# Kernel tuning notes

Measured on AMD Instinct MI355X. Metric: run time of the kernel, lower is better.

## Reference

```python
import jax, jax.numpy as jnp
import numpy as np

B, S, C, OUT = 8, 2048, 1024, 1024

def setup_inputs() -> dict:
    key = jax.random.key(0)
    ks = jax.random.split(key, 10)
    s = C ** -0.5
    return {
        "input": jax.random.normal(ks[0], (B, S, C), jnp.float32),
        "memory": jax.random.normal(ks[1], (B, S, C), jnp.float32),
        "Wq": jax.random.normal(ks[2], (C, C), jnp.float32) * s,
        "bq": jnp.zeros((C,), jnp.float32),
        "Wk": jax.random.normal(ks[3], (C, C), jnp.float32) * s,
        "bk": jnp.zeros((C,), jnp.float32),
        "Wv": jax.random.normal(ks[4], (C, C), jnp.float32) * s,
        "bv": jnp.zeros((C,), jnp.float32),
        "Wo": jax.random.normal(ks[5], (OUT, C), jnp.float32) * s,
        "bo": jnp.zeros((OUT,), jnp.float32),
    }

def reference(input, memory, Wq, bq, Wk, bk, Wv, bv, Wo, bo):
    depth_scale = input.shape[2] ** -0.5
    q = (input @ Wq.T + bq) * depth_scale          # [B, Sq, C]
    k = memory @ Wk.T + bk                          # [B, Sk, C]
    v = memory @ Wv.T + bv                          # [B, Sk, C]
    logit = jnp.einsum('bqc,bkc->bqk', q, k)        # [B, Sq, Sk]
    attn = jax.nn.softmax(logit, axis=-1)
    sel = jnp.einsum('bqk,bkc->bqc', attn, v)       # [B, Sq, C]
    return sel @ Wo.T + bo                          # [B, Sq, OUT]
```

## Files before the change

### kernel.cpp

```cpp
#include <hip/hip_runtime.h>
#include <hip/hip_bf16.h>


typedef __attribute__((ext_vector_type(8))) short short8;
typedef __attribute__((ext_vector_type(4))) float f32x4;

static __device__ __forceinline__ unsigned short f2bf(float f) {
  union { float f; unsigned u; } x; x.f = f;
  unsigned r = x.u + 0x7FFFu + ((x.u >> 16) & 1u);
  return (unsigned short)(r >> 16);
}

static __device__ __forceinline__ long long brickoff(int r_, int k_, int Kd) {
  return (long long)(r_ >> 7) * ((long long)128 * Kd) +
         (long long)(k_ >> 5) * 4096 +
         (r_ & 127) * 32 +
         (((((k_ >> 3) & 3) ^ ((r_ >> 1) & 3))) << 3) +
         (k_ & 7);
}

__global__ __launch_bounds__(256) void cvt_brick_kernel(
    const float* __restrict__ s0, const float* __restrict__ s1,
    unsigned short* __restrict__ o0, unsigned short* __restrict__ o1,
    long long ngran) {
  const float* src = blockIdx.y ? s1 : s0;
  unsigned short* dst = blockIdx.y ? o1 : o0;
  long long gid = (long long)blockIdx.x * 256 + threadIdx.x;
  const long long stride = (long long)gridDim.x * 256;
  for (; gid < ngran; gid += stride) {
    const int tile = (int)(gid >> 14);
    const int g2 = (int)(gid & 16383);
    const int ks = g2 >> 9;
    const int rp = g2 & 511;
    const int r = rp >> 2;
    const int p = rp & 3;
    const int g = p ^ ((r >> 1) & 3);
    const float* sp = src + (long long)(tile * 128 + r) * 1024 + ks * 32 + g * 8;
    float4 u0 = ((const float4*)sp)[0];
    float4 u1 = ((const float4*)sp)[1];
    short8 pk;
    pk[0] = (short)f2bf(u0.x); pk[1] = (short)f2bf(u0.y);
    pk[2] = (short)f2bf(u0.z); pk[3] = (short)f2bf(u0.w);
    pk[4] = (short)f2bf(u1.x); pk[5] = (short)f2bf(u1.y);
    pk[6] = (short)f2bf(u1.z); pk[7] = (short)f2bf(u1.w);
    *(short8*)&dst[gid * 8] = pk;
  }
}

__global__ __launch_bounds__(256) void wcvt_brick_kernel(
    const float* __restrict__ w0, const float* __restrict__ w1,
    const float* __restrict__ w2, const float* __restrict__ w3,
    unsigned short* __restrict__ o0, unsigned short* __restrict__ o1,
    unsigned short* __restrict__ o2, unsigned short* __restrict__ o3) {
  const float* src; unsigned short* dst;
  switch (blockIdx.y) {
    case 0: src = w0; dst = o0; break;
    case 1: src = w1; dst = o1; break;
    case 2: src = w2; dst = o2; break;
    default: src = w3; dst = o3; break;
  }
  const int gid = blockIdx.x * 256 + threadIdx.x;
  const int tile = gid >> 14;
  const int g2 = gid & 16383;
  const int ks = g2 >> 9;
  const int rp = g2 & 511;
  const int r = rp >> 2;
  const int p = rp & 3;
  const int g = p ^ ((r >> 1) & 3);
  const float* sp = src + (long long)(tile * 128 + r) * 1024 + ks * 32 + g * 8;
  float4 u0 = ((const float4*)sp)[0];
  float4 u1 = ((const float4*)sp)[1];
  short8 pk;
  pk[0] = (short)f2bf(u0.x); pk[1] = (short)f2bf(u0.y);
  pk[2] = (short)f2bf(u0.z); pk[3] = (short)f2bf(u0.w);
  pk[4] = (short)f2bf(u1.x); pk[5] = (short)f2bf(u1.y);
  pk[6] = (short)f2bf(u1.z); pk[7] = (short)f2bf(u1.w);
  *(short8*)&dst[(long long)gid * 8] = pk;
}

#define EPI_BF16 0
#define EPI_BF16_TRANS 1
#define EPI_EXP 2
#define EPI_PV 3
#define EPI_F32 4

template <int MFR, int NFR, int EPI, bool HAS_BIAS>
__global__ __launch_bounds__(256, (MFR * NFR >= 32) ? 2 : 3) void gemm_kernel(
    const unsigned short* __restrict__ A, const unsigned short* __restrict__ B,
    const float* __restrict__ bias, void* __restrict__ Dv,
    int NT, int ldaK, int ldbK, int ldd,
    long long sA, long long sBflat, int sBslice, int kOffB,
    long long sD, float scale) {
  constexpr int BM = MFR * 32;
  constexpr int BN = NFR * 32;

  int i = blockIdx.x + gridDim.x * (blockIdx.y + gridDim.y * blockIdx.z);
  const int nwg = gridDim.x * gridDim.y * gridDim.z;
  int v = (i & 7) * (nwg >> 3) + (i >> 3);
  const int by = v % gridDim.y;
  int u = v / gridDim.y;
  const int bx = u % gridDim.x;
  const int bz = u / gridDim.x;

  const int bm = bx * BM;
  const int bn = by * BN;
  const int tid = threadIdx.x;
  const int lane = tid & 63;
  const int wid = tid >> 6;
  const int wr = (wid >> 1) * (MFR * 16);
  const int wc = (wid & 1) * (NFR * 16);
  const int fr = lane & 15;
  const int hi = lane >> 4;
  const int laneoff = fr * 32 + ((hi ^ ((fr >> 1) & 3)) << 3);

  f32x4 acc[MFR][NFR];
#pragma unroll
  for (int m = 0; m < MFR; ++m)
#pragma unroll
    for (int n = 0; n < NFR; ++n) acc[m][n] = (f32x4){0.f, 0.f, 0.f, 0.f};

  f32x4 asum[MFR];
  short8 ones;
#pragma unroll
  for (int m = 0; m < MFR; ++m) asum[m] = (f32x4){0.f, 0.f, 0.f, 0.f};
#pragma unroll
  for (int j = 0; j < 8; ++j) ones[j] = (short)0x3F80;

  const unsigned short* Ap = A + bz * sA +
      (long long)((bm + wr) >> 7) * 128 * ldaK + (wr & 127) * 32 + laneoff;
  const unsigned short* Bp = B + bz * sBflat +
      (long long)((bn + wc) >> 7) * 128 * ldbK +
      (long long)(kOffB + bz * sBslice) * 4096 + (wc & 127) * 32 + laneoff;

  short8 a0[MFR], b0[NFR], a1[MFR], b1[NFR];
  auto LDA = [&](short8 (&d)[MFR], int t) {
    const unsigned short* p = Ap + (long long)t * 4096;
#pragma unroll
    for (int m = 0; m < MFR; ++m) d[m] = *(const short8*)(p + m * 512);
  };
  auto LDB = [&](short8 (&d)[NFR], int t) {
    const unsigned short* p = Bp + (long long)t * 4096;
#pragma unroll
    for (int n = 0; n < NFR; ++n) d[n] = *(const short8*)(p + n * 512);
  };
  auto FMA = [&](short8 (&a)[MFR], short8 (&b)[NFR]) {
#pragma unroll
    for (int m = 0; m < MFR; ++m)
#pragma unroll
      for (int n = 0; n < NFR; ++n)
        acc[m][n] = __builtin_amdgcn_mfma_f32_16x16x32_bf16(a[m], b[n],
                                                            acc[m][n], 0, 0, 0);
    if (EPI == EPI_PV) {
#pragma unroll
      for (int m = 0; m < MFR; ++m)
        asum[m] = __builtin_amdgcn_mfma_f32_16x16x32_bf16(a[m], ones,
                                                          asum[m], 0, 0, 0);
    }
  };

  LDA(a0, 0); LDB(b0, 0);
  LDA(a1, 1); LDB(b1, 1);
  for (int t = 0; t < NT - 2; t += 2) {
    FMA(a0, b0);
    LDA(a0, t + 2); LDB(b0, t + 2);
    FMA(a1, b1);
    LDA(a1, t + 3); LDB(b1, t + 3);
  }
  FMA(a0, b0);
  FMA(a1, b1);

  const int cr = hi * 4;
  const int cc = fr;
#pragma unroll
  for (int m = 0; m < MFR; ++m) {
    const int row0 = bm + wr + m * 16 + cr;
#pragma unroll
    for (int n = 0; n < NFR; ++n) {
      const int col = bn + wc + n * 16 + cc;
      const float bv = HAS_BIAS ? bias[col] : 0.f;
      if (EPI == EPI_F32) {
        float* D = (float*)Dv + bz * sD;
#pragma unroll
        for (int j = 0; j < 4; ++j)
          D[(long long)(row0 + j) * ldd + col] = acc[m][n][j] + bv;
      } else if (EPI == EPI_BF16) {
        unsigned short* D = (unsigned short*)Dv + bz * sD;
#pragma unroll
        for (int j = 0; j < 4; ++j)
          D[brickoff(row0 + j, col, ldd)] = f2bf((acc[m][n][j] + bv) * scale);
      } else if (EPI == EPI_BF16_TRANS) {
        unsigned short* D = (unsigned short*)Dv + bz * sD;
#pragma unroll
        for (int j = 0; j < 4; ++j)
          D[brickoff(col, row0 + j, ldd)] = f2bf((acc[m][n][j] + bv) * scale);
      } else if (EPI == EPI_EXP) {
        unsigned short* D = (unsigned short*)Dv + bz * sD;
#pragma unroll
        for (int j = 0; j < 4; ++j)
          D[brickoff(row0 + j, col, ldd)] = f2bf(__expf(acc[m][n][j]));
      } else {
        unsigned short* D = (unsigned short*)Dv + bz * sD;
#pragma unroll
        for (int j = 0; j < 4; ++j) {
          const float li = 1.f / asum[m][j];
          D[brickoff(row0 + j, col, ldd)] = f2bf(acc[m][n][j] * li);
        }
      }
    }
  }
}

extern "C" void kernel_launch(void* const* d_in, const int* in_sizes, int n_in,
                              void* d_out, int out_size, void* d_ws, size_t ws_size,
                              hipStream_t stream) {
  (void)in_sizes; (void)n_in; (void)out_size;
  const float* input  = (const float*)d_in[0];
  const float* memory = (const float*)d_in[1];
  const float* Wq = (const float*)d_in[2];
  const float* bq = (const float*)d_in[3];
  const float* Wk = (const float*)d_in[4];
  const float* bk = (const float*)d_in[5];
  const float* Wv = (const float*)d_in[6];
  const float* bv = (const float*)d_in[7];
  const float* Wo = (const float*)d_in[8];
  const float* bo = (const float*)d_in[9];
  float* out = (float*)d_out;

  const int S = 2048, C = 1024;
  const int CB = 4;
  const long long BS = 16384;
  const long long N_IN = BS * C;
  const long long N_W  = (long long)C * C;

  char* p = (char*)d_ws;
  auto alloc = [&](size_t bytes) {
    char* r = p;
    p += (bytes + 255) & ~(size_t)255;
    return r;
  };
  unsigned short* wqb  = (unsigned short*)alloc(N_W * 2);
  unsigned short* wkb  = (unsigned short*)alloc(N_W * 2);
  unsigned short* wvb  = (unsigned short*)alloc(N_W * 2);
  unsigned short* wob  = (unsigned short*)alloc(N_W * 2);
  unsigned short* Qb   = (unsigned short*)alloc(N_IN * 2);
  unsigned short* Kb   = (unsigned short*)alloc(N_IN * 2);
  unsigned short* Xb   = (unsigned short*)alloc(N_IN * 2);
  if ((size_t)(p - (char*)d_ws) > ws_size) return;

  unsigned short* Vt  = (unsigned short*)d_out;
  unsigned short* inb = (unsigned short*)d_out + N_IN;
  unsigned short* memb = Xb;
  unsigned short* Pt   = Xb;

  wcvt_brick_kernel<<<dim3(512, 4, 1), 256, 0, stream>>>(Wq, Wk, Wv, Wo,
                                                         wqb, wkb, wvb, wob);
  cvt_brick_kernel<<<dim3(2048, 2, 1), 256, 0, stream>>>(memory, input, memb, inb,
                                                         N_IN / 8);

  const float depth_scale = 0.03125f;

  gemm_kernel<4, 8, EPI_BF16, true><<<dim3(128, 4, 1), 256, 0, stream>>>(
      memb, wkb, bk, Kb, 32, C, C, C, 0, 0, 0, 0, 0, 1.0f);
  gemm_kernel<4, 8, EPI_BF16_TRANS, true><<<dim3(128, 4, 1), 256, 0, stream>>>(
      memb, wvb, bv, Vt, 32, C, C, (int)BS, 0, 0, 0, 0, 0, 1.0f);
  gemm_kernel<4, 8, EPI_BF16, true><<<dim3(128, 4, 1), 256, 0, stream>>>(
      inb, wqb, bq, Qb, 32, C, C, C, 0, 0, 0, 0, 0, depth_scale);

  for (int c = 0; c < 8 / CB; ++c) {
    const long long qoff = (long long)c * CB * S * C;
    gemm_kernel<4, 8, EPI_EXP, false><<<dim3(16, 8, CB), 256, 0, stream>>>(
        Qb + qoff, Kb + qoff, nullptr, Pt,
        32, C, C, S, (long long)S * C, (long long)S * C, 0, 0,
        (long long)S * S, 1.0f);
    gemm_kernel<4, 4, EPI_PV, false><<<dim3(16, 8, CB), 256, 0, stream>>>(
        Pt, Vt, nullptr, Qb + qoff,
        64, S, (int)BS, C, (long long)S * S, 0, 64, c * CB * 64,
        (long long)S * C, 1.0f);
  }

  gemm_kernel<4, 8, EPI_F32, true><<<dim3(128, 4, 1), 256, 0, stream>>>(
      Qb, wob, bo, out, 32, C, C, C, 0, 0, 0, 0, 0, 1.0f);
}
```

Before: 378.9 us.

## Add supertile block swizzle and triple-buffered register prefetch in GEMM

```diff
diff --git a/kernel.cpp b/kernel.cpp
--- a/kernel.cpp
+++ b/kernel.cpp
@@ -84,7 +84,7 @@
 #define EPI_PV 3
 #define EPI_F32 4
 
-template <int MFR, int NFR, int EPI, bool HAS_BIAS>
+template <int MFR, int NFR, int EPI, bool HAS_BIAS, int SX, int SY>
 __global__ __launch_bounds__(256, (MFR * NFR >= 32) ? 2 : 3) void gemm_kernel(
     const unsigned short* __restrict__ A, const unsigned short* __restrict__ B,
     const float* __restrict__ bias, void* __restrict__ Dv,
@@ -96,11 +96,16 @@
 
   int i = blockIdx.x + gridDim.x * (blockIdx.y + gridDim.y * blockIdx.z);
   const int nwg = gridDim.x * gridDim.y * gridDim.z;
-  int v = (i & 7) * (nwg >> 3) + (i >> 3);
-  const int by = v % gridDim.y;
-  int u = v / gridDim.y;
-  const int bx = u % gridDim.x;
-  const int bz = u / gridDim.x;
+  const int v = (i & 7) * (nwg >> 3) + (i >> 3);
+  const int gx = gridDim.x, gy = gridDim.y;
+  const int pb = gx * gy;
+  const int bz = v / pb;
+  const int r0 = v % pb;
+  const int nsx = gx / SX;
+  const int st = r0 / (SX * SY);
+  const int w0 = r0 % (SX * SY);
+  const int bx = (st % nsx) * SX + (w0 % SX);
+  const int by = (st / nsx) * SY + (w0 / SX);
 
   const int bm = bx * BM;
   const int bn = by * BN;
@@ -127,12 +132,12 @@
   for (int j = 0; j < 8; ++j) ones[j] = (short)0x3F80;
 
   const unsigned short* Ap = A + bz * sA +
-      (long long)((bm + wr) >> 7) * 128 * ldaK + (wr & 127) * 32 + laneoff;
+      (long long)((bm + wr) >> 7) * 128 * ldaK + ((bm + wr) & 127) * 32 + laneoff;
   const unsigned short* Bp = B + bz * sBflat +
       (long long)((bn + wc) >> 7) * 128 * ldbK +
-      (long long)(kOffB + bz * sBslice) * 4096 + (wc & 127) * 32 + laneoff;
-
-  short8 a0[MFR], b0[NFR], a1[MFR], b1[NFR];
+      (long long)(kOffB + bz * sBslice) * 4096 + ((bn + wc) & 127) * 32 + laneoff;
+
+  short8 a0[MFR], b0[NFR], a1[MFR], b1[NFR], a2[MFR], b2[NFR];
   auto LDA = [&](short8 (&d)[MFR], int t) {
     const unsigned short* p = Ap + (long long)t * 4096;
 #pragma unroll
@@ -160,14 +165,18 @@
 
   LDA(a0, 0); LDB(b0, 0);
   LDA(a1, 1); LDB(b1, 1);
-  for (int t = 0; t < NT - 2; t += 2) {
+  LDA(a2, 2); LDB(b2, 2);
+  int t = 0;
+  for (; t + 3 <= NT; t += 3) {
     FMA(a0, b0);
-    LDA(a0, t + 2); LDB(b0, t + 2);
+    if (t + 3 < NT) { LDA(a0, t + 3); LDB(b0, t + 3); }
     FMA(a1, b1);
-    LDA(a1, t + 3); LDB(b1, t + 3);
-  }
-  FMA(a0, b0);
-  FMA(a1, b1);
+    if (t + 4 < NT) { LDA(a1, t + 4); LDB(b1, t + 4); }
+    FMA(a2, b2);
+    if (t + 5 < NT) { LDA(a2, t + 5); LDB(b2, t + 5); }
+  }
+  if (t < NT) { FMA(a0, b0); ++t; }
+  if (t < NT) { FMA(a1, b1); ++t; }
 
   const int cr = hi * 4;
   const int cc = fr;
@@ -259,25 +268,25 @@
 
   const float depth_scale = 0.03125f;
 
-  gemm_kernel<4, 8, EPI_BF16, true><<<dim3(128, 4, 1), 256, 0, stream>>>(
+  gemm_kernel<4, 8, EPI_BF16, true, 8, 4><<<dim3(128, 4, 1), 256, 0, stream>>>(
       memb, wkb, bk, Kb, 32, C, C, C, 0, 0, 0, 0, 0, 1.0f);
-  gemm_kernel<4, 8, EPI_BF16_TRANS, true><<<dim3(128, 4, 1), 256, 0, stream>>>(
+  gemm_kernel<4, 8, EPI_BF16_TRANS, true, 8, 4><<<dim3(128, 4, 1), 256, 0, stream>>>(
       memb, wvb, bv, Vt, 32, C, C, (int)BS, 0, 0, 0, 0, 0, 1.0f);
-  gemm_kernel<4, 8, EPI_BF16, true><<<dim3(128, 4, 1), 256, 0, stream>>>(
+  gemm_kernel<4, 8, EPI_BF16, true, 8, 4><<<dim3(128, 4, 1), 256, 0, stream>>>(
       inb, wqb, bq, Qb, 32, C, C, C, 0, 0, 0, 0, 0, depth_scale);
 
   for (int c = 0; c < 8 / CB; ++c) {
     const long long qoff = (long long)c * CB * S * C;
-    gemm_kernel<4, 8, EPI_EXP, false><<<dim3(16, 8, CB), 256, 0, stream>>>(
+    gemm_kernel<4, 8, EPI_EXP, false, 8, 4><<<dim3(16, 8, CB), 256, 0, stream>>>(
         Qb + qoff, Kb + qoff, nullptr, Pt,
         32, C, C, S, (long long)S * C, (long long)S * C, 0, 0,
         (long long)S * S, 1.0f);
-    gemm_kernel<4, 4, EPI_PV, false><<<dim3(16, 8, CB), 256, 0, stream>>>(
+    gemm_kernel<4, 4, EPI_PV, false, 4, 4><<<dim3(16, 8, CB), 256, 0, stream>>>(
         Pt, Vt, nullptr, Qb + qoff,
         64, S, (int)BS, C, (long long)S * S, 0, 64, c * CB * 64,
         (long long)S * C, 1.0f);
   }
 
-  gemm_kernel<4, 8, EPI_F32, true><<<dim3(128, 4, 1), 256, 0, stream>>>(
+  gemm_kernel<4, 8, EPI_F32, true, 8, 4><<<dim3(128, 4, 1), 256, 0, stream>>>(
       Qb, wob, bo, out, 32, C, C, C, 0, 0, 0, 0, 0, 1.0f);
 }
```

Result: slower. 1.254 ms (+230.9%).
